# Performance work log

Hardware: AMD Instinct MI355X
Metric: run time of the kernel (lower is better)

The kernel has to match this reference:

```python
import jax, jax.numpy as jnp
import numpy as np
from jax import lax

TWN_THRESHOLD_FACTOR = 0.05


def ternary_quantize(w, t):
    # codes in {-1, 0, +1}
    return (w > t).astype(w.dtype) - (w < -t).astype(w.dtype)


def setup_inputs() -> dict:
    key = jax.random.key(0)
    kx, kw, kb = jax.random.split(key, 3)
    x = jax.random.normal(kx, (32, 128, 56, 56), dtype=jnp.float32)
    weight = jax.random.normal(kw, (256, 128, 3, 3), dtype=jnp.float32)
    bias = jax.random.normal(kb, (256,), dtype=jnp.float32)
    return {"x": x, "weight": weight, "bias": bias}


def reference(x, weight, bias):
    # threshold from detached weights (matches weight.detach().abs().max())
    threshold = TWN_THRESHOLD_FACTOR * jnp.max(jnp.abs(lax.stop_gradient(weight)))
    q_weight = ternary_quantize(weight, threshold)
    out = lax.conv_general_dilated(
        x, q_weight,
        window_strides=(1, 1),
        padding="VALID",  # F.conv2d default padding=0
        dimension_numbers=("NCHW", "OIHW", "NCHW"),
    )
    return out + bias[None, :, None, None]
```

## Files before the change

kernel.cpp:

```cpp
#include <hip/hip_runtime.h>
#include <hip/hip_bf16.h>
#include <stdint.h>

#define NB   32
#define CIN  128
#define HIN  56
#define WIN  56
#define KOUT 256
#define HOUT 54
#define WOUT 54
#define PQ   (HOUT*WOUT)
#define NPIX (NB*PQ)
#define KK   (CIN*9)
#define HW   (HIN*WIN)
#define TWN_FACTOR 0.05f

typedef short bf16x8 __attribute__((ext_vector_type(8)));
typedef float f32x4  __attribute__((ext_vector_type(4)));

__device__ __forceinline__ void glds16(const void* g, void* l) {
  __builtin_amdgcn_global_load_lds(
      (__attribute__((address_space(1))) void*)(g),
      (__attribute__((address_space(3))) void*)(l),
      16, 0, 0);
}

__global__ void prep_k(const float* __restrict__ x, const float4* __restrict__ w4,
                       float* __restrict__ amax, __hip_bfloat16* __restrict__ xt) {
  __shared__ __hip_bfloat16 tl[64 * 130 + 32];
  __shared__ float sm[4];
  int bid = blockIdx.x;
  int t   = threadIdx.x;

  if (bid < 288) {
    float4 v = w4[bid * 256 + t];
    float m = fmaxf(fmaxf(fabsf(v.x), fabsf(v.y)), fmaxf(fabsf(v.z), fabsf(v.w)));
    #pragma unroll
    for (int off = 32; off > 0; off >>= 1)
      m = fmaxf(m, __shfl_down(m, off));
    int lane = t & 63, wv = t >> 6;
    if (lane == 0) sm[wv] = m;
    __syncthreads();
    if (t == 0)
      atomicMax(amax, fmaxf(fmaxf(sm[0], sm[1]), fmaxf(sm[2], sm[3])));
    return;
  }

  int b2 = bid - 288;
  int n  = b2 / 49, pc = b2 - n * 49;
  const float* xb = x + (size_t)n * CIN * HW + pc * 64;
  int f4 = t & 15, c0 = t >> 4;
  #pragma unroll
  for (int rd = 0; rd < 8; ++rd) {
    int c = c0 + rd * 16;
    float4 v = *(const float4*)(xb + (size_t)c * HW + f4 * 4);
    tl[(f4 * 4 + 0) * 130 + c] = __float2bfloat16(v.x);
    tl[(f4 * 4 + 1) * 130 + c] = __float2bfloat16(v.y);
    tl[(f4 * 4 + 2) * 130 + c] = __float2bfloat16(v.z);
    tl[(f4 * 4 + 3) * 130 + c] = __float2bfloat16(v.w);
  }
  __syncthreads();
  int cc = t & 15, p0 = t >> 4;
  __hip_bfloat16* op = xt + ((size_t)n * HW + pc * 64) * CIN + cc * 8;
  #pragma unroll
  for (int p = p0; p < 64; p += 16)
    *(bf16x8*)(op + (size_t)p * CIN) = *(const bf16x8*)&tl[p * 130 + cc * 8];
}

__global__ void quant_k(const float* __restrict__ w, const float* __restrict__ amax,
                        __hip_bfloat16* __restrict__ qA) {
  float thr = TWN_FACTOR * (*amax);
  int t  = blockIdx.x * 256 + threadIdx.x;
  int kc = t >> 8, row = t & 255;
  int rs = kc >> 4, c0 = (kc & 15) << 3;
  bf16x8 q;
  #pragma unroll
  for (int j = 0; j < 8; ++j) {
    float v  = w[(size_t)(row * CIN + c0 + j) * 9 + rs];
    float qq = (v > thr) ? 1.f : ((v < -thr) ? -1.f : 0.f);
    q[j] = (short)__bfloat16_as_ushort(__float2bfloat16(qq));
  }
  *(bf16x8*)(qA + (size_t)t * 8) = q;
}

__global__ __launch_bounds__(256) void conv_gemm(
    const __hip_bfloat16* __restrict__ xt,
    const __hip_bfloat16* __restrict__ qA,
    const float* __restrict__ bias,
    float* __restrict__ out) {
  __shared__ __hip_bfloat16 Bs[2][128 * 64];

  const int tid  = threadIdx.x;
  const int wave = tid >> 6;
  const int lane = tid & 63;
  const int quad = lane >> 4;
  const int l16  = lane & 15;

  const int orig = blockIdx.x;
  const int xcd  = orig & 7;
  const int loc  = orig >> 3;
  const int bid  = (xcd < 2) ? xcd * 183 + loc
                             : 366 + (xcd - 2) * 182 + loc;

  const int ktile = bid & 1;
  const int ptile = bid >> 1;
  const int k0    = ktile * 128;
  const int pbase = ptile * 128;

  const int wm = (wave >> 1) * 64;
  const int wn = (wave & 1) * 64;

  const int r8 = lane >> 3;
  const int ch = lane & 7;
  unsigned boffm[4];
  #pragma unroll
  for (int m = 0; m < 4; ++m) {
    int row  = wave * 32 + m * 8 + r8;
    int prow = pbase + row;
    int n = prow / PQ; int rm = prow - n * PQ;
    int p = rm / WOUT; int q = rm - p * WOUT;
    boffm[m] = (unsigned)(n * HW + p * WIN + q) * CIN + ((ch ^ (row & 7)) << 3);
  }

  unsigned aoff[4];
  #pragma unroll
  for (int i = 0; i < 4; ++i)
    aoff[i] = (unsigned)(quad * 256 + (k0 + wm + i * 16 + l16)) * 8;

  f32x4 acc[4][4];
  #pragma unroll
  for (int i = 0; i < 4; ++i)
    #pragma unroll
    for (int j = 0; j < 4; ++j)
      acc[i][j] = (f32x4){0.f, 0.f, 0.f, 0.f};

  {
    char* bdst = (char*)Bs[0] + wave * 4096;
    #pragma unroll
    for (int m = 0; m < 4; ++m)
      glds16(xt + boffm[m], bdst + m * 1024);
  }
  __syncthreads();

  #pragma unroll
  for (int t = 0; t < 18; ++t) {
    const unsigned astep = ((unsigned)(t >> 1) * 16 + (unsigned)(t & 1) * 8) * 2048;

    bf16x8 af[2][4];
    #pragma unroll
    for (int h = 0; h < 2; ++h)
      #pragma unroll
      for (int i = 0; i < 4; ++i)
        af[h][i] = *(const bf16x8*)(qA + aoff[i] + astep + (unsigned)h * 4 * 2048);

    if (t < 17) {
      const int tn  = t + 1;
      const int rsn = tn >> 1;
      const int rn  = rsn / 3, sn = rsn - rn * 3;
      const unsigned bst = (unsigned)((rn * WIN + sn) * CIN + (tn & 1) * 64);
      char* bdst = (char*)Bs[tn & 1] + wave * 4096;
      #pragma unroll
      for (int m = 0; m < 4; ++m)
        glds16(xt + boffm[m] + bst, bdst + m * 1024);
    }

    const char* bp = (const char*)Bs[t & 1];
    #pragma unroll
    for (int h = 0; h < 2; ++h) {
      bf16x8 bfr[4];
      #pragma unroll
      for (int i = 0; i < 4; ++i) {
        int row = wn + i * 16 + l16;
        bfr[i] = *(const bf16x8*)(bp + (row * 64 + (((h * 4 + quad) ^ (row & 7)) << 3)) * 2);
      }
      #pragma unroll
      for (int i = 0; i < 4; ++i)
        #pragma unroll
        for (int j = 0; j < 4; ++j)
          acc[i][j] = __builtin_amdgcn_mfma_f32_16x16x32_bf16(af[h][i], bfr[j], acc[i][j], 0, 0, 0);
    }
    __syncthreads();
  }

  const float4* b4 = (const float4*)bias;
  #pragma unroll
  for (int j = 0; j < 4; ++j) {
    int pix  = pbase + wn + j * 16 + l16;
    int nimg = pix / PQ;
    int pq   = pix - nimg * PQ;
    size_t obase = (size_t)nimg * (KOUT * PQ) + pq;
    #pragma unroll
    for (int i = 0; i < 4; ++i) {
      int kb = k0 + wm + i * 16 + quad * 4;
      float4 bv = b4[kb >> 2];
      out[obase + (size_t)(kb + 0) * PQ] = acc[i][j][0] + bv.x;
      out[obase + (size_t)(kb + 1) * PQ] = acc[i][j][1] + bv.y;
      out[obase + (size_t)(kb + 2) * PQ] = acc[i][j][2] + bv.z;
      out[obase + (size_t)(kb + 3) * PQ] = acc[i][j][3] + bv.w;
    }
  }
}

extern "C" void kernel_launch(void* const* d_in, const int* in_sizes, int n_in,
                              void* d_out, int out_size, void* d_ws, size_t ws_size,
                              hipStream_t stream) {
  const float* x    = (const float*)d_in[0];
  const float* w    = (const float*)d_in[1];
  const float* bias = (const float*)d_in[2];
  float* out = (float*)d_out;

  float* amax = (float*)d_ws;
  __hip_bfloat16* xt = (__hip_bfloat16*)((char*)d_ws + 256);
  __hip_bfloat16* qA = (__hip_bfloat16*)((char*)d_ws + 256 + (size_t)NB * HW * CIN * 2);

  prep_k  <<<dim3(1856), dim3(256), 0, stream>>>(x, (const float4*)w, amax, xt);
  quant_k <<<dim3(144),  dim3(256), 0, stream>>>(w, amax, qA);
  conv_gemm<<<dim3(1458), dim3(256), 0, stream>>>(xt, qA, bias, out);
}
```

Before: 212.7 us.

## Triple-buffer conv GEMM B tiles and stage epilogue through LDS for vector stores

Result: faster. 196.2 us (-7.7%).

```diff
diff --git a/kernel.cpp b/kernel.cpp
--- a/kernel.cpp
+++ b/kernel.cpp
@@ -83,12 +83,12 @@
   *(bf16x8*)(qA + (size_t)t * 8) = q;
 }
 
-__global__ __launch_bounds__(256) void conv_gemm(
+__global__ __launch_bounds__(256, 3) void conv_gemm(
     const __hip_bfloat16* __restrict__ xt,
     const __hip_bfloat16* __restrict__ qA,
     const float* __restrict__ bias,
     float* __restrict__ out) {
-  __shared__ __hip_bfloat16 Bs[2][128 * 64];
+  __shared__ __hip_bfloat16 Bs[3][128 * 64];
 
   const int tid  = threadIdx.x;
   const int wave = tid >> 6;
@@ -135,15 +135,22 @@
       acc[i][j] = (f32x4){0.f, 0.f, 0.f, 0.f};
 
   {
-    char* bdst = (char*)Bs[0] + wave * 4096;
+    char* bdst0 = (char*)Bs + wave * 4096;
     #pragma unroll
     for (int m = 0; m < 4; ++m)
-      glds16(xt + boffm[m], bdst + m * 1024);
-  }
-  __syncthreads();
+      glds16(xt + boffm[m], bdst0 + m * 1024);
+    char* bdst1 = (char*)Bs + 16384 + wave * 4096;
+    #pragma unroll
+    for (int m = 0; m < 4; ++m)
+      glds16(xt + boffm[m] + 64u, bdst1 + m * 1024);
+  }
 
   #pragma unroll
   for (int t = 0; t < 18; ++t) {
+    asm volatile("s_waitcnt vmcnt(4)" ::: "memory");
+    __builtin_amdgcn_s_barrier();
+    __builtin_amdgcn_sched_barrier(0);
+
     const unsigned astep = ((unsigned)(t >> 1) * 16 + (unsigned)(t & 1) * 8) * 2048;
 
     bf16x8 af[2][4];
@@ -152,19 +159,20 @@
       #pragma unroll
       for (int i = 0; i < 4; ++i)
         af[h][i] = *(const bf16x8*)(qA + aoff[i] + astep + (unsigned)h * 4 * 2048);
-
-    if (t < 17) {
-      const int tn  = t + 1;
+    __builtin_amdgcn_sched_barrier(0);
+
+    if (t < 16) {
+      const int tn  = t + 2;
       const int rsn = tn >> 1;
       const int rn  = rsn / 3, sn = rsn - rn * 3;
       const unsigned bst = (unsigned)((rn * WIN + sn) * CIN + (tn & 1) * 64);
-      char* bdst = (char*)Bs[tn & 1] + wave * 4096;
+      char* bdst = (char*)Bs + (unsigned)(tn % 3) * 16384 + wave * 4096;
       #pragma unroll
       for (int m = 0; m < 4; ++m)
         glds16(xt + boffm[m] + bst, bdst + m * 1024);
     }
 
-    const char* bp = (const char*)Bs[t & 1];
+    const char* bp = (const char*)Bs + (unsigned)(t % 3) * 16384;
     #pragma unroll
     for (int h = 0; h < 2; ++h) {
       bf16x8 bfr[4];
@@ -179,24 +187,44 @@
         for (int j = 0; j < 4; ++j)
           acc[i][j] = __builtin_amdgcn_mfma_f32_16x16x32_bf16(af[h][i], bfr[j], acc[i][j], 0, 0, 0);
     }
-    __syncthreads();
-  }
-
-  const float4* b4 = (const float4*)bias;
-  #pragma unroll
-  for (int j = 0; j < 4; ++j) {
-    int pix  = pbase + wn + j * 16 + l16;
-    int nimg = pix / PQ;
-    int pq   = pix - nimg * PQ;
-    size_t obase = (size_t)nimg * (KOUT * PQ) + pq;
+  }
+
+  __syncthreads();
+
+  {
+    float* Sw = (float*)Bs + wave * 2048;
+    const int ST  = 65;
+    const int rk  = lane >> 3;
+    const int rp  = (lane & 7) * 4;
+    const float4* b4 = (const float4*)bias;
+
     #pragma unroll
     for (int i = 0; i < 4; ++i) {
-      int kb = k0 + wm + i * 16 + quad * 4;
-      float4 bv = b4[kb >> 2];
-      out[obase + (size_t)(kb + 0) * PQ] = acc[i][j][0] + bv.x;
-      out[obase + (size_t)(kb + 1) * PQ] = acc[i][j][1] + bv.y;
-      out[obase + (size_t)(kb + 2) * PQ] = acc[i][j][2] + bv.z;
-      out[obase + (size_t)(kb + 3) * PQ] = acc[i][j][3] + bv.w;
+      float4 bv = b4[(k0 + wm + i * 16 + quad * 4) >> 2];
+      #pragma unroll
+      for (int j = 0; j < 4; ++j) {
+        Sw[(quad * 4 + 0) * ST + j * 16 + l16] = acc[i][j][0] + bv.x;
+        Sw[(quad * 4 + 1) * ST + j * 16 + l16] = acc[i][j][1] + bv.y;
+        Sw[(quad * 4 + 2) * ST + j * 16 + l16] = acc[i][j][2] + bv.z;
+        Sw[(quad * 4 + 3) * ST + j * 16 + l16] = acc[i][j][3] + bv.w;
+      }
+      asm volatile("s_waitcnt lgkmcnt(0)" ::: "memory");
+      __builtin_amdgcn_sched_barrier(0);
+      #pragma unroll
+      for (int ri = 0; ri < 2; ++ri) {
+        int klocal = ri * 8 + rk;
+        int k = k0 + wm + i * 16 + klocal;
+        #pragma unroll
+        for (int cg = 0; cg < 2; ++cg) {
+          int pixl = cg * 32 + rp;
+          float4 v = *(const float4*)&Sw[klocal * ST + pixl];
+          int pix = pbase + wn + pixl;
+          int n = pix / PQ, pq = pix - n * PQ;
+          *(float4*)(out + (size_t)n * (KOUT * PQ) + (size_t)k * PQ + pq) = v;
+        }
+      }
+      asm volatile("s_waitcnt lgkmcnt(0)" ::: "memory");
+      __builtin_amdgcn_sched_barrier(0);
     }
   }
 }
```
